# Kernel tuning notes

Hardware: AMD Instinct MI355X
Metric: run time of the kernel (lower is better)

The kernel has to match this reference:

```python
import jax, jax.numpy as jnp
import numpy as np

N = 50000          # nodes
E = 1_600_000      # edges (avg degree 32)
F_IN = 512         # input feature dim
H = 256            # hidden_channels
C = 121            # num_classes (PPI)
L = 4              # num_layers
ALPHA = 0.5
THETA = 1.0


def setup_inputs() -> dict:
    key = jax.random.key(0)
    ks = jax.random.split(key, 8)
    x = jax.random.normal(ks[0], (N, F_IN), jnp.float32)
    edge_src = jax.random.randint(ks[1], (E,), 0, N, jnp.int32)
    edge_dst = jax.random.randint(ks[2], (E,), 0, N, jnp.int32)
    edge_weight = jax.random.uniform(ks[3], (E,), jnp.float32)
    s0 = 1.0 / np.sqrt(F_IN).astype(np.float32)
    lin0_w = jax.random.uniform(ks[4], (F_IN, H), jnp.float32, -s0, s0)
    lin0_b = jnp.zeros((H,), jnp.float32)
    conv_ws = jax.random.normal(ks[5], (L, H, H), jnp.float32) / np.float32(np.sqrt(H))
    s1 = 1.0 / np.sqrt(H).astype(np.float32)
    lin1_w = jax.random.uniform(ks[6], (H, C), jnp.float32, -s1, s1)
    lin1_b = jnp.zeros((C,), jnp.float32)
    return {
        "x": x, "edge_src": edge_src, "edge_dst": edge_dst,
        "edge_weight": edge_weight, "lin0_w": lin0_w, "lin0_b": lin0_b,
        "conv_ws": conv_ws, "lin1_w": lin1_w, "lin1_b": lin1_b,
    }


def reference(x, edge_src, edge_dst, edge_weight, lin0_w, lin0_b, conv_ws, lin1_w, lin1_b):
    # input projection + relu (dropout p=0 -> identity)
    x = jax.nn.relu(x @ lin0_w + lin0_b)          # [N, H]
    x0 = x
    for layer in range(L):
        beta = np.float32(np.log(THETA / (layer + 1) + 1.0))
        # sparse propagation: h = A @ x  (edge-wise gather * weight, scatter-add)
        msg = x[edge_src] * edge_weight[:, None]   # [E, H]
        h = jax.ops.segment_sum(msg, edge_dst, num_segments=N)  # [N, H]
        # GCN2Conv (shared_weights=True, normalize=False)
        h = (1.0 - ALPHA) * h + ALPHA * x0
        h = (1.0 - beta) * h + beta * (h @ conv_ws[layer])
        # residual + relu
        x = jax.nn.relu(h + x)
    return x @ lin1_w + lin1_b                    # [N, C]
```

## Files before the change

### kernel.cpp

```cpp
#include <hip/hip_runtime.h>
#include <math.h>

#define N_NODES 50000
#define E_EDGES 1600000
#define F_INDIM 512
#define H_DIM   256
#define C_OUT   121
#define L_LAYERS 4

typedef unsigned short u16;
typedef short bf16x8 __attribute__((ext_vector_type(8)));
typedef float f32x4  __attribute__((ext_vector_type(4)));

__device__ __forceinline__ float bf2f(u16 h) {
    return __uint_as_float(((unsigned int)h) << 16);
}
__device__ __forceinline__ u16 f2bf(float f) {
    unsigned int u = __float_as_uint(f);
    unsigned int r = u + 0x7FFFu + ((u >> 16) & 1u);
    return (u16)(r >> 16);
}

__global__ void zeroi_kernel(int* __restrict__ p, int n) {
    int i = blockIdx.x * blockDim.x + threadIdx.x;
    if (i < n) p[i] = 0;
}

__global__ void transpose_kernel(const float* __restrict__ W, u16* __restrict__ WT,
                                 int K, int N, int NPAD) {
    int i = blockIdx.x * blockDim.x + threadIdx.x;
    if (i >= NPAD * K) return;
    int n = i / K, k = i - n * K;
    WT[(long)n * K + k] = (n < N) ? f2bf(W[(long)k * N + n]) : (u16)0;
}

__global__ void hist_kernel(const int* __restrict__ dst, int* __restrict__ deg) {
    int e = blockIdx.x * blockDim.x + threadIdx.x;
    if (e < E_EDGES) {
        int d = dst[e];
        if (d >= 0 && d < N_NODES) atomicAdd(&deg[d], 1);
    }
}

__global__ void scan_kernel(const int* __restrict__ deg, int* __restrict__ row_ptr) {
    __shared__ int sums[256];
    const int t = threadIdx.x;
    const int CH = (N_NODES + 255) / 256;
    const int base = t * CH;
    int s = 0;
    for (int i = 0; i < CH; ++i) {
        int idx = base + i;
        if (idx < N_NODES) s += deg[idx];
    }
    sums[t] = s;
    __syncthreads();
    for (int off = 1; off < 256; off <<= 1) {
        int v = (t >= off) ? sums[t - off] : 0;
        __syncthreads();
        sums[t] += v;
        __syncthreads();
    }
    int run = (t == 0) ? 0 : sums[t - 1];
    for (int i = 0; i < CH; ++i) {
        int idx = base + i;
        if (idx < N_NODES) { row_ptr[idx] = run; run += deg[idx]; }
    }
    if (t == 255) row_ptr[N_NODES] = run;
}

__global__ void scatter_kernel(const int* __restrict__ src, const int* __restrict__ dst,
                               const float* __restrict__ w, const int* __restrict__ row_ptr,
                               int* __restrict__ cnt, int* __restrict__ s_src,
                               float* __restrict__ s_w) {
    int e = blockIdx.x * blockDim.x + threadIdx.x;
    if (e < E_EDGES) {
        int d = dst[e];
        if (d < 0) d = 0; if (d >= N_NODES) d = N_NODES - 1;
        int p = atomicAdd(&cnt[d], 1);
        long idx = (long)row_ptr[d] + p;
        if (idx < 0) idx = 0; if (idx >= E_EDGES) idx = E_EDGES - 1;
        s_src[idx] = src[e];
        s_w[idx]   = w[e];
    }
}

__global__ __launch_bounds__(256) void layer_kernel(
        const int* __restrict__ row_ptr, const int* __restrict__ s_src,
        const float* __restrict__ s_w, const u16* __restrict__ Xin,
        const u16* __restrict__ X0, u16* __restrict__ Xout,
        const u16* __restrict__ WT, float beta) {
    __shared__ __align__(16) u16 hs[16 * H_DIM];
    const int w  = threadIdx.x >> 6;
    const int l  = threadIdx.x & 63;
    const int hi = l >> 4, lo = l & 15;
    const int half = l >> 5;
    const int q    = l & 31;
    const int bm = blockIdx.x * 16;

    for (int i = 0; i < 4; ++i) {
        const int rl  = w * 4 + i;
        const int row = bm + rl;
        int beg = row_ptr[row], end = row_ptr[row + 1];
        if (beg < 0) beg = 0; if (end > E_EDGES) end = E_EDGES;
        float accA[8] = {}, accB[8] = {};
        for (int e = beg; e < end; e += 4) {
            const int eA = e + half;
            const int eB = e + 2 + half;
            const int cA = (eA < end) ? eA : end - 1;
            const int cB = (eB < end) ? eB : end - 1;
            float wA = (eA < end) ? s_w[cA] : 0.f;
            float wB = (eB < end) ? s_w[cB] : 0.f;
            int sA = s_src[cA]; if (sA < 0) sA = 0; if (sA >= N_NODES) sA = N_NODES - 1;
            int sB = s_src[cB]; if (sB < 0) sB = 0; if (sB >= N_NODES) sB = N_NODES - 1;
            bf16x8 vA = *reinterpret_cast<const bf16x8*>(Xin + (long)sA * H_DIM + q * 8);
            bf16x8 vB = *reinterpret_cast<const bf16x8*>(Xin + (long)sB * H_DIM + q * 8);
            #pragma unroll
            for (int j = 0; j < 8; ++j) {
                accA[j] += wA * bf2f((u16)vA[j]);
                accB[j] += wB * bf2f((u16)vB[j]);
            }
        }
        if (l < 32) {
        }
        float acc[8];
        #pragma unroll
        for (int j = 0; j < 8; ++j) {
            float s = accA[j] + accB[j];
            s += __shfl_xor(s, 32);
            acc[j] = s;
        }
        if (l < 32) {
            bf16x8 x0 = *reinterpret_cast<const bf16x8*>(X0 + (long)row * H_DIM + q * 8);
            bf16x8 ov;
            #pragma unroll
            for (int j = 0; j < 8; ++j)
                ov[j] = (short)f2bf(0.5f * acc[j] + 0.5f * bf2f((u16)x0[j]));
            const int off = rl * 512 + ((q * 16) ^ ((rl & 7) << 4));
            *reinterpret_cast<bf16x8*>((char*)hs + off) = ov;
        }
    }
    __syncthreads();

    const int col0 = w * 64;
    f32x4 acc[4];
    #pragma unroll
    for (int t = 0; t < 4; ++t) acc[t] = (f32x4){0.f, 0.f, 0.f, 0.f};

    for (int k0 = 0; k0 < H_DIM; k0 += 32) {
        const int aoff = lo * 512 + (((k0 * 2) + hi * 16) ^ ((lo & 7) << 4));
        bf16x8 a = *reinterpret_cast<const bf16x8*>((const char*)hs + aoff);
        #pragma unroll
        for (int t = 0; t < 4; ++t) {
            bf16x8 b = *reinterpret_cast<const bf16x8*>(
                    WT + (long)(col0 + t * 16 + lo) * H_DIM + k0 + hi * 8);
            acc[t] = __builtin_amdgcn_mfma_f32_16x16x32_bf16(a, b, acc[t], 0, 0, 0);
        }
    }

    #pragma unroll
    for (int t = 0; t < 4; ++t) {
        const int col = col0 + t * 16 + lo;
        #pragma unroll
        for (int r = 0; r < 4; ++r) {
            const int rl  = hi * 4 + r;
            const int row = bm + rl;
            const int hoff = rl * 512 + ((col * 2) ^ ((rl & 7) << 4));
            float hv = bf2f(*reinterpret_cast<const u16*>((const char*)hs + hoff));
            long idx = (long)row * H_DIM + col;
            float v = (1.f - beta) * hv + beta * acc[t][r] + bf2f(Xin[idx]);
            Xout[idx] = f2bf(fmaxf(v, 0.f));
        }
    }
}

template <int K, int NT, int MODE>
__global__ __launch_bounds__(256) void mfma_gemm_kernel(
        const void* __restrict__ Aptr, const u16* __restrict__ WT,
        const float* __restrict__ bias,
        u16* __restrict__ X, u16* __restrict__ X0, float* __restrict__ out) {
    const int w  = threadIdx.x >> 6;
    const int l  = threadIdx.x & 63;
    const int hi = l >> 4, lo = l & 15;
    const int bm = blockIdx.x * 16;
    const int col0 = w * (NT * 16);

    f32x4 acc[NT];
    #pragma unroll
    for (int t = 0; t < NT; ++t) acc[t] = (f32x4){0.f, 0.f, 0.f, 0.f};

    for (int k0 = 0; k0 < K; k0 += 32) {
        bf16x8 a;
        if (MODE == 0) {
            const float* ap = (const float*)Aptr + (long)(bm + lo) * K + k0 + hi * 8;
            float4 f0 = *reinterpret_cast<const float4*>(ap);
            float4 f1 = *reinterpret_cast<const float4*>(ap + 4);
            a[0] = (short)f2bf(f0.x); a[1] = (short)f2bf(f0.y);
            a[2] = (short)f2bf(f0.z); a[3] = (short)f2bf(f0.w);
            a[4] = (short)f2bf(f1.x); a[5] = (short)f2bf(f1.y);
            a[6] = (short)f2bf(f1.z); a[7] = (short)f2bf(f1.w);
        } else {
            a = *reinterpret_cast<const bf16x8*>(
                    (const u16*)Aptr + (long)(bm + lo) * K + k0 + hi * 8);
        }
        #pragma unroll
        for (int t = 0; t < NT; ++t) {
            bf16x8 b = *reinterpret_cast<const bf16x8*>(
                    WT + (long)(col0 + t * 16 + lo) * K + k0 + hi * 8);
            acc[t] = __builtin_amdgcn_mfma_f32_16x16x32_bf16(a, b, acc[t], 0, 0, 0);
        }
    }

    #pragma unroll
    for (int t = 0; t < NT; ++t) {
        const int col = col0 + t * 16 + lo;
        #pragma unroll
        for (int r = 0; r < 4; ++r) {
            const int row = bm + hi * 4 + r;
            float v = acc[t][r];
            if (MODE == 0) {
                v = fmaxf(v + bias[col], 0.f);
                u16 h = f2bf(v);
                long idx = (long)row * H_DIM + col;
                X[idx] = h; X0[idx] = h;
            } else {
                if (col < C_OUT) out[(long)row * C_OUT + col] = v + bias[col];
            }
        }
    }
}

extern "C" void kernel_launch(void* const* d_in, const int* in_sizes, int n_in,
                              void* d_out, int out_size, void* d_ws, size_t ws_size,
                              hipStream_t stream) {
    const float* x_in = (const float*)d_in[0];
    const int*   esrc = (const int*)d_in[1];
    const int*   edst = (const int*)d_in[2];
    const float* ew   = (const float*)d_in[3];
    const float* l0w  = (const float*)d_in[4];
    const float* l0b  = (const float*)d_in[5];
    const float* cw   = (const float*)d_in[6];
    const float* l1w  = (const float*)d_in[7];
    const float* l1b  = (const float*)d_in[8];
    float* out = (float*)d_out;
    (void)in_sizes; (void)n_in; (void)out_size;

    char* ws = (char*)d_ws;
    auto al = [](size_t x) { return (x + 255) & ~(size_t)255; };
    size_t o = 0;
    const size_t NHb = (size_t)N_NODES * H_DIM * sizeof(u16);
    u16* Xa = (u16*)(ws + o);  o += al(NHb);
    u16* Xb = (u16*)(ws + o);  o += al(NHb);
    u16* X0 = (u16*)(ws + o);  o += al(NHb);
    int* row_ptr = (int*)(ws + o); o += al((N_NODES + 1) * sizeof(int));
    int* cnt     = (int*)(ws + o); o += al((size_t)N_NODES * sizeof(int));
    int* s_src   = (int*)(ws + o); o += al((size_t)E_EDGES * sizeof(int));
    float* s_w   = (float*)(ws + o); o += al((size_t)E_EDGES * sizeof(float));
    u16* WT0 = (u16*)(ws + o); o += al((size_t)H_DIM * F_INDIM * sizeof(u16));
    u16* WTc = (u16*)(ws + o); o += al((size_t)L_LAYERS * H_DIM * H_DIM * sizeof(u16));
    u16* WT1 = (u16*)(ws + o); o += al((size_t)128 * H_DIM * sizeof(u16));
    if (ws_size < o) return;

    const int MBLK = N_NODES / 16;

    transpose_kernel<<<(H_DIM * F_INDIM + 255) / 256, 256, 0, stream>>>(
        l0w, WT0, F_INDIM, H_DIM, H_DIM);
    for (int l = 0; l < L_LAYERS; ++l)
        transpose_kernel<<<(H_DIM * H_DIM + 255) / 256, 256, 0, stream>>>(
            cw + (size_t)l * H_DIM * H_DIM, WTc + (size_t)l * H_DIM * H_DIM,
            H_DIM, H_DIM, H_DIM);
    transpose_kernel<<<(128 * H_DIM + 255) / 256, 256, 0, stream>>>(
        l1w, WT1, H_DIM, C_OUT, 128);

    mfma_gemm_kernel<F_INDIM, 4, 0><<<MBLK, 256, 0, stream>>>(
        x_in, WT0, l0b, Xa, X0, nullptr);

    zeroi_kernel<<<(N_NODES + 255) / 256, 256, 0, stream>>>(cnt, N_NODES);
    hist_kernel<<<(E_EDGES + 255) / 256, 256, 0, stream>>>(edst, cnt);
    scan_kernel<<<1, 256, 0, stream>>>(cnt, row_ptr);
    zeroi_kernel<<<(N_NODES + 255) / 256, 256, 0, stream>>>(cnt, N_NODES);
    scatter_kernel<<<(E_EDGES + 255) / 256, 256, 0, stream>>>(esrc, edst, ew, row_ptr,
                                                              cnt, s_src, s_w);

    u16* Xcur = Xa;
    u16* Xnxt = Xb;
    for (int l = 0; l < L_LAYERS; ++l) {
        float beta = logf(1.0f / (float)(l + 1) + 1.0f);
        layer_kernel<<<MBLK, 256, 0, stream>>>(row_ptr, s_src, s_w, Xcur, X0, Xnxt,
                                               WTc + (size_t)l * H_DIM * H_DIM, beta);
        u16* tmp = Xcur; Xcur = Xnxt; Xnxt = tmp;
    }

    mfma_gemm_kernel<H_DIM, 2, 2><<<MBLK, 256, 0, stream>>>(
        Xcur, WT1, l1b, nullptr, nullptr, out);
}
```

Measured before the change: 1.124 ms.

## Pack CSR edge src/weight into int2 and gather 4 rows per half-wave

The separate s_src and s_w arrays become one interleaved int2 array, so each edge needs a single 8-byte load instead of two scattered 4-byte loads. The aggregation loop now handles 8 edges per iteration, with each half-wave issuing 4 independent row gathers before accumulating into one register set. The aim is more memory-level parallelism on the latency-bound neighbour gathers and fewer index-load instructions, at the cost of more registers and more wasted lanes on low-degree tails.

```diff
diff --git a/kernel.cpp b/kernel.cpp
--- a/kernel.cpp
+++ b/kernel.cpp
@@ -70,8 +70,7 @@
 
 __global__ void scatter_kernel(const int* __restrict__ src, const int* __restrict__ dst,
                                const float* __restrict__ w, const int* __restrict__ row_ptr,
-                               int* __restrict__ cnt, int* __restrict__ s_src,
-                               float* __restrict__ s_w) {
+                               int* __restrict__ cnt, int2* __restrict__ eidx) {
     int e = blockIdx.x * blockDim.x + threadIdx.x;
     if (e < E_EDGES) {
         int d = dst[e];
@@ -79,14 +78,13 @@
         int p = atomicAdd(&cnt[d], 1);
         long idx = (long)row_ptr[d] + p;
         if (idx < 0) idx = 0; if (idx >= E_EDGES) idx = E_EDGES - 1;
-        s_src[idx] = src[e];
-        s_w[idx]   = w[e];
+        eidx[idx] = make_int2(src[e], __float_as_int(w[e]));
     }
 }
 
 __global__ __launch_bounds__(256) void layer_kernel(
-        const int* __restrict__ row_ptr, const int* __restrict__ s_src,
-        const float* __restrict__ s_w, const u16* __restrict__ Xin,
+        const int* __restrict__ row_ptr, const int2* __restrict__ eidx,
+        const u16* __restrict__ Xin,
         const u16* __restrict__ X0, u16* __restrict__ Xout,
         const u16* __restrict__ WT, float beta) {
     __shared__ __align__(16) u16 hs[16 * H_DIM];
@@ -102,30 +100,35 @@
         const int row = bm + rl;
         int beg = row_ptr[row], end = row_ptr[row + 1];
         if (beg < 0) beg = 0; if (end > E_EDGES) end = E_EDGES;
-        float accA[8] = {}, accB[8] = {};
-        for (int e = beg; e < end; e += 4) {
-            const int eA = e + half;
-            const int eB = e + 2 + half;
-            const int cA = (eA < end) ? eA : end - 1;
-            const int cB = (eB < end) ? eB : end - 1;
-            float wA = (eA < end) ? s_w[cA] : 0.f;
-            float wB = (eB < end) ? s_w[cB] : 0.f;
-            int sA = s_src[cA]; if (sA < 0) sA = 0; if (sA >= N_NODES) sA = N_NODES - 1;
-            int sB = s_src[cB]; if (sB < 0) sB = 0; if (sB >= N_NODES) sB = N_NODES - 1;
-            bf16x8 vA = *reinterpret_cast<const bf16x8*>(Xin + (long)sA * H_DIM + q * 8);
-            bf16x8 vB = *reinterpret_cast<const bf16x8*>(Xin + (long)sB * H_DIM + q * 8);
-            #pragma unroll
-            for (int j = 0; j < 8; ++j) {
-                accA[j] += wA * bf2f((u16)vA[j]);
-                accB[j] += wB * bf2f((u16)vB[j]);
-            }
-        }
-        if (l < 32) {
+        float acc8[8] = {};
+        for (int e = beg; e < end; e += 8) {
+            const int b0 = e + half * 4;
+            int2 m[4];
+            #pragma unroll
+            for (int u = 0; u < 4; ++u) {
+                const int eu = b0 + u;
+                m[u] = eidx[(eu < end) ? eu : end - 1];
+                if (eu >= end) m[u].y = 0;
+            }
+            bf16x8 v[4];
+            #pragma unroll
+            for (int u = 0; u < 4; ++u) {
+                int s = m[u].x;
+                if (s < 0) s = 0; if (s >= N_NODES) s = N_NODES - 1;
+                v[u] = *reinterpret_cast<const bf16x8*>(Xin + (long)s * H_DIM + q * 8);
+            }
+            #pragma unroll
+            for (int u = 0; u < 4; ++u) {
+                const float wt = __int_as_float(m[u].y);
+                #pragma unroll
+                for (int j = 0; j < 8; ++j)
+                    acc8[j] += wt * bf2f((u16)v[u][j]);
+            }
         }
         float acc[8];
         #pragma unroll
         for (int j = 0; j < 8; ++j) {
-            float s = accA[j] + accB[j];
+            float s = acc8[j];
             s += __shfl_xor(s, 32);
             acc[j] = s;
         }
@@ -253,8 +256,7 @@
     u16* X0 = (u16*)(ws + o);  o += al(NHb);
     int* row_ptr = (int*)(ws + o); o += al((N_NODES + 1) * sizeof(int));
     int* cnt     = (int*)(ws + o); o += al((size_t)N_NODES * sizeof(int));
-    int* s_src   = (int*)(ws + o); o += al((size_t)E_EDGES * sizeof(int));
-    float* s_w   = (float*)(ws + o); o += al((size_t)E_EDGES * sizeof(float));
+    int2* eidx   = (int2*)(ws + o); o += al((size_t)E_EDGES * sizeof(int2));
     u16* WT0 = (u16*)(ws + o); o += al((size_t)H_DIM * F_INDIM * sizeof(u16));
     u16* WTc = (u16*)(ws + o); o += al((size_t)L_LAYERS * H_DIM * H_DIM * sizeof(u16));
     u16* WT1 = (u16*)(ws + o); o += al((size_t)128 * H_DIM * sizeof(u16));
@@ -279,13 +281,13 @@
     scan_kernel<<<1, 256, 0, stream>>>(cnt, row_ptr);
     zeroi_kernel<<<(N_NODES + 255) / 256, 256, 0, stream>>>(cnt, N_NODES);
     scatter_kernel<<<(E_EDGES + 255) / 256, 256, 0, stream>>>(esrc, edst, ew, row_ptr,
-                                                              cnt, s_src, s_w);
+                                                              cnt, eidx);
 
     u16* Xcur = Xa;
     u16* Xnxt = Xb;
     for (int l = 0; l < L_LAYERS; ++l) {
         float beta = logf(1.0f / (float)(l + 1) + 1.0f);
-        layer_kernel<<<MBLK, 256, 0, stream>>>(row_ptr, s_src, s_w, Xcur, X0, Xnxt,
+        layer_kernel<<<MBLK, 256, 0, stream>>>(row_ptr, eidx, Xcur, X0, Xnxt,
                                                WTc + (size_t)l * H_DIM * H_DIM, beta);
         u16* tmp = Xcur; Xcur = Xnxt; Xnxt = tmp;
     }
```

After: 1.158 ms. 3.0% more time.

## Fuse final projection into last layer kernel and merge weight prep launches

Applied to the files above, without the earlier changes.

Merges six weight transpose launches into one prep kernel. The scan now writes its prefix offsets into the count array, so the scatter can use them as atomic cursors and the second zeroing pass goes away. The last GCN layer keeps its output tile in shared memory and runs the final 256x121 projection with MFMA, writing the result directly. This removes the final GEMM launch and a full write and read of the layer output, at the cost of extra shared memory and a branchier layer kernel.

```diff
diff --git a/kernel.cpp b/kernel.cpp
--- a/kernel.cpp
+++ b/kernel.cpp
@@ -26,12 +26,26 @@
     if (i < n) p[i] = 0;
 }
 
-__global__ void transpose_kernel(const float* __restrict__ W, u16* __restrict__ WT,
-                                 int K, int N, int NPAD) {
+__global__ void prep_kernel(const float* __restrict__ l0w, const float* __restrict__ cw,
+                            const float* __restrict__ l1w, u16* __restrict__ WT0,
+                            u16* __restrict__ WTc, u16* __restrict__ WT1) {
     int i = blockIdx.x * blockDim.x + threadIdx.x;
-    if (i >= NPAD * K) return;
-    int n = i / K, k = i - n * K;
-    WT[(long)n * K + k] = (n < N) ? f2bf(W[(long)k * N + n]) : (u16)0;
+    if (i < 131072) {
+        int n = i >> 9, k = i & 511;
+        WT0[i] = f2bf(l0w[(long)k * H_DIM + n]);
+        return;
+    }
+    i -= 131072;
+    if (i < 262144) {
+        int l = i >> 16, j = i & 65535, n = j >> 8, k = j & 255;
+        WTc[(l << 16) + j] = f2bf(cw[(long)l * 65536 + (long)k * H_DIM + n]);
+        return;
+    }
+    i -= 262144;
+    if (i < 32768) {
+        int n = i >> 8, k = i & 255;
+        WT1[i] = (n < C_OUT) ? f2bf(l1w[(long)k * C_OUT + n]) : (u16)0;
+    }
 }
 
 __global__ void hist_kernel(const int* __restrict__ dst, int* __restrict__ deg) {
@@ -42,7 +56,7 @@
     }
 }
 
-__global__ void scan_kernel(const int* __restrict__ deg, int* __restrict__ row_ptr) {
+__global__ void scan_kernel(int* cnt, int* __restrict__ row_ptr) {
     __shared__ int sums[256];
     const int t = threadIdx.x;
     const int CH = (N_NODES + 255) / 256;
@@ -50,7 +64,7 @@
     int s = 0;
     for (int i = 0; i < CH; ++i) {
         int idx = base + i;
-        if (idx < N_NODES) s += deg[idx];
+        if (idx < N_NODES) s += cnt[idx];
     }
     sums[t] = s;
     __syncthreads();
@@ -63,21 +77,25 @@
     int run = (t == 0) ? 0 : sums[t - 1];
     for (int i = 0; i < CH; ++i) {
         int idx = base + i;
-        if (idx < N_NODES) { row_ptr[idx] = run; run += deg[idx]; }
+        if (idx < N_NODES) {
+            int dv = cnt[idx];
+            row_ptr[idx] = run;
+            cnt[idx] = run;
+            run += dv;
+        }
     }
     if (t == 255) row_ptr[N_NODES] = run;
 }
 
 __global__ void scatter_kernel(const int* __restrict__ src, const int* __restrict__ dst,
-                               const float* __restrict__ w, const int* __restrict__ row_ptr,
+                               const float* __restrict__ w,
                                int* __restrict__ cnt, int* __restrict__ s_src,
                                float* __restrict__ s_w) {
     int e = blockIdx.x * blockDim.x + threadIdx.x;
     if (e < E_EDGES) {
         int d = dst[e];
         if (d < 0) d = 0; if (d >= N_NODES) d = N_NODES - 1;
-        int p = atomicAdd(&cnt[d], 1);
-        long idx = (long)row_ptr[d] + p;
+        long idx = atomicAdd(&cnt[d], 1);
         if (idx < 0) idx = 0; if (idx >= E_EDGES) idx = E_EDGES - 1;
         s_src[idx] = src[e];
         s_w[idx]   = w[e];
@@ -88,8 +106,11 @@
         const int* __restrict__ row_ptr, const int* __restrict__ s_src,
         const float* __restrict__ s_w, const u16* __restrict__ Xin,
         const u16* __restrict__ X0, u16* __restrict__ Xout,
-        const u16* __restrict__ WT, float beta) {
+        const u16* __restrict__ WT, float beta,
+        const u16* __restrict__ WT1, const float* __restrict__ l1b,
+        float* __restrict__ outp) {
     __shared__ __align__(16) u16 hs[16 * H_DIM];
+    __shared__ __align__(16) u16 xs[16 * H_DIM];
     const int w  = threadIdx.x >> 6;
     const int l  = threadIdx.x & 63;
     const int hi = l >> 4, lo = l & 15;
@@ -120,8 +141,6 @@
                 accB[j] += wB * bf2f((u16)vB[j]);
             }
         }
-        if (l < 32) {
-        }
         float acc[8];
         #pragma unroll
         for (int j = 0; j < 8; ++j) {
@@ -168,16 +187,51 @@
             float hv = bf2f(*reinterpret_cast<const u16*>((const char*)hs + hoff));
             long idx = (long)row * H_DIM + col;
             float v = (1.f - beta) * hv + beta * acc[t][r] + bf2f(Xin[idx]);
-            Xout[idx] = f2bf(fmaxf(v, 0.f));
-        }
-    }
-}
-
-template <int K, int NT, int MODE>
+            u16 vb = f2bf(fmaxf(v, 0.f));
+            if (outp == nullptr) {
+                Xout[idx] = vb;
+            } else {
+                *reinterpret_cast<u16*>((char*)xs + hoff) = vb;
+            }
+        }
+    }
+
+    if (outp != nullptr) {
+        __syncthreads();
+        const int c1 = w * 32;
+        f32x4 acc2[2];
+        acc2[0] = (f32x4){0.f, 0.f, 0.f, 0.f};
+        acc2[1] = (f32x4){0.f, 0.f, 0.f, 0.f};
+        for (int k0 = 0; k0 < H_DIM; k0 += 32) {
+            const int aoff = lo * 512 + (((k0 * 2) + hi * 16) ^ ((lo & 7) << 4));
+            bf16x8 a = *reinterpret_cast<const bf16x8*>((const char*)xs + aoff);
+            #pragma unroll
+            for (int t = 0; t < 2; ++t) {
+                bf16x8 b = *reinterpret_cast<const bf16x8*>(
+                        WT1 + (long)(c1 + t * 16 + lo) * H_DIM + k0 + hi * 8);
+                acc2[t] = __builtin_amdgcn_mfma_f32_16x16x32_bf16(a, b, acc2[t], 0, 0, 0);
+            }
+        }
+        #pragma unroll
+        for (int t = 0; t < 2; ++t) {
+            const int col = c1 + t * 16 + lo;
+            if (col < C_OUT) {
+                const float bias = l1b[col];
+                #pragma unroll
+                for (int r = 0; r < 4; ++r) {
+                    const int row = bm + hi * 4 + r;
+                    outp[(long)row * C_OUT + col] = acc2[t][r] + bias;
+                }
+            }
+        }
+    }
+}
+
+template <int K, int NT>
 __global__ __launch_bounds__(256) void mfma_gemm_kernel(
-        const void* __restrict__ Aptr, const u16* __restrict__ WT,
+        const float* __restrict__ Aptr, const u16* __restrict__ WT,
         const float* __restrict__ bias,
-        u16* __restrict__ X, u16* __restrict__ X0, float* __restrict__ out) {
+        u16* __restrict__ X, u16* __restrict__ X0) {
     const int w  = threadIdx.x >> 6;
     const int l  = threadIdx.x & 63;
     const int hi = l >> 4, lo = l & 15;
@@ -190,18 +244,13 @@
 
     for (int k0 = 0; k0 < K; k0 += 32) {
         bf16x8 a;
-        if (MODE == 0) {
-            const float* ap = (const float*)Aptr + (long)(bm + lo) * K + k0 + hi * 8;
-            float4 f0 = *reinterpret_cast<const float4*>(ap);
-            float4 f1 = *reinterpret_cast<const float4*>(ap + 4);
-            a[0] = (short)f2bf(f0.x); a[1] = (short)f2bf(f0.y);
-            a[2] = (short)f2bf(f0.z); a[3] = (short)f2bf(f0.w);
-            a[4] = (short)f2bf(f1.x); a[5] = (short)f2bf(f1.y);
-            a[6] = (short)f2bf(f1.z); a[7] = (short)f2bf(f1.w);
-        } else {
-            a = *reinterpret_cast<const bf16x8*>(
-                    (const u16*)Aptr + (long)(bm + lo) * K + k0 + hi * 8);
-        }
+        const float* ap = Aptr + (long)(bm + lo) * K + k0 + hi * 8;
+        float4 f0 = *reinterpret_cast<const float4*>(ap);
+        float4 f1 = *reinterpret_cast<const float4*>(ap + 4);
+        a[0] = (short)f2bf(f0.x); a[1] = (short)f2bf(f0.y);
+        a[2] = (short)f2bf(f0.z); a[3] = (short)f2bf(f0.w);
+        a[4] = (short)f2bf(f1.x); a[5] = (short)f2bf(f1.y);
+        a[6] = (short)f2bf(f1.z); a[7] = (short)f2bf(f1.w);
         #pragma unroll
         for (int t = 0; t < NT; ++t) {
             bf16x8 b = *reinterpret_cast<const bf16x8*>(
@@ -216,15 +265,10 @@
         #pragma unroll
         for (int r = 0; r < 4; ++r) {
             const int row = bm + hi * 4 + r;
-            float v = acc[t][r];
-            if (MODE == 0) {
-                v = fmaxf(v + bias[col], 0.f);
-                u16 h = f2bf(v);
-                long idx = (long)row * H_DIM + col;
-                X[idx] = h; X0[idx] = h;
-            } else {
-                if (col < C_OUT) out[(long)row * C_OUT + col] = v + bias[col];
-            }
+            float v = fmaxf(acc[t][r] + bias[col], 0.f);
+            u16 h = f2bf(v);
+            long idx = (long)row * H_DIM + col;
+            X[idx] = h; X0[idx] = h;
         }
     }
 }
@@ -262,34 +306,25 @@
 
     const int MBLK = N_NODES / 16;
 
-    transpose_kernel<<<(H_DIM * F_INDIM + 255) / 256, 256, 0, stream>>>(
-        l0w, WT0, F_INDIM, H_DIM, H_DIM);
-    for (int l = 0; l < L_LAYERS; ++l)
-        transpose_kernel<<<(H_DIM * H_DIM + 255) / 256, 256, 0, stream>>>(
-            cw + (size_t)l * H_DIM * H_DIM, WTc + (size_t)l * H_DIM * H_DIM,
-            H_DIM, H_DIM, H_DIM);
-    transpose_kernel<<<(128 * H_DIM + 255) / 256, 256, 0, stream>>>(
-        l1w, WT1, H_DIM, C_OUT, 128);
-
-    mfma_gemm_kernel<F_INDIM, 4, 0><<<MBLK, 256, 0, stream>>>(
-        x_in, WT0, l0b, Xa, X0, nullptr);
+    prep_kernel<<<1664, 256, 0, stream>>>(l0w, cw, l1w, WT0, WTc, WT1);
+
+    mfma_gemm_kernel<F_INDIM, 4><<<MBLK, 256, 0, stream>>>(x_in, WT0, l0b, Xa, X0);
 
     zeroi_kernel<<<(N_NODES + 255) / 256, 256, 0, stream>>>(cnt, N_NODES);
     hist_kernel<<<(E_EDGES + 255) / 256, 256, 0, stream>>>(edst, cnt);
     scan_kernel<<<1, 256, 0, stream>>>(cnt, row_ptr);
-    zeroi_kernel<<<(N_NODES + 255) / 256, 256, 0, stream>>>(cnt, N_NODES);
-    scatter_kernel<<<(E_EDGES + 255) / 256, 256, 0, stream>>>(esrc, edst, ew, row_ptr,
+    scatter_kernel<<<(E_EDGES + 255) / 256, 256, 0, stream>>>(esrc, edst, ew,
                                                               cnt, s_src, s_w);
 
     u16* Xcur = Xa;
     u16* Xnxt = Xb;
     for (int l = 0; l < L_LAYERS; ++l) {
         float beta = logf(1.0f / (float)(l + 1) + 1.0f);
-        layer_kernel<<<MBLK, 256, 0, stream>>>(row_ptr, s_src, s_w, Xcur, X0, Xnxt,
-                                               WTc + (size_t)l * H_DIM * H_DIM, beta);
+        const bool last = (l == L_LAYERS - 1);
+        layer_kernel<<<MBLK, 256, 0, stream>>>(
+            row_ptr, s_src, s_w, Xcur, X0, Xnxt,
+            WTc + (size_t)l * H_DIM * H_DIM, beta,
+            last ? WT1 : nullptr, last ? l1b : nullptr, last ? out : nullptr);
         u16* tmp = Xcur; Xcur = Xnxt; Xnxt = tmp;
     }
-
-    mfma_gemm_kernel<H_DIM, 2, 2><<<MBLK, 256, 0, stream>>>(
-        Xcur, WT1, l1b, nullptr, nullptr, out);
-}
+}
```

Measured after the change: 1.183 ms. 5.2% more time.
